# Optimization experiments

Measured on AMD Instinct MI355X. Metric: run time of the kernel, lower is better.

## Reference

```python
import jax, jax.numpy as jnp
import numpy as np

B, H, W, C = 4, 192, 640, 32
S = 32
STEPS = np.arange(S, dtype=np.float32)  # depth steps (init kwarg 'steps')


def setup_inputs() -> dict:
    key = jax.random.key(0)
    k1, k2, k3, k4, k5 = jax.random.split(key, 5)
    x = jax.random.normal(k1, (B, H, W, C), jnp.float32)
    y = jax.random.normal(k2, (B, H, W, C), jnp.float32)
    # principal point near image center, focal ~500px, small translation T12
    origin = jnp.array([[W / 2.0, H / 2.0]], jnp.float32) + jax.random.uniform(k3, (B, 2), jnp.float32)
    focal = 500.0 + 50.0 * jax.random.uniform(k4, (B, 2), jnp.float32)
    T12 = 0.01 * jax.random.normal(k5, (B, 3), jnp.float32)
    return {"x": x, "y": y, "origin": origin, "focal": focal, "T12": T12}


def _bilinear_1img(img, sx, sy):
    # img [H,W,C]; sx [W]: source x-coord for each output column; sy [H]: source y per row.
    # Matches tf.contrib.image.transform BILINEAR with fill value 0 outside the image.
    x0 = jnp.floor(sx); fx = sx - x0
    y0 = jnp.floor(sy); fy = sy - y0
    x0i = x0.astype(jnp.int32); x1i = x0i + 1
    y0i = y0.astype(jnp.int32); y1i = y0i + 1
    mx0 = ((x0i >= 0) & (x0i < W)).astype(img.dtype)
    mx1 = ((x1i >= 0) & (x1i < W)).astype(img.dtype)
    my0 = ((y0i >= 0) & (y0i < H)).astype(img.dtype)
    my1 = ((y1i >= 0) & (y1i < H)).astype(img.dtype)
    # interpolate along y first (transform is separable: x'=a*x+b, y'=a*y+c)
    r0 = img[jnp.clip(y0i, 0, H - 1)]                     # [H,W,C]
    r1 = img[jnp.clip(y1i, 0, H - 1)]                     # [H,W,C]
    rows = (my0 * (1.0 - fy))[:, None, None] * r0 + (my1 * fy)[:, None, None] * r1
    c0 = rows[:, jnp.clip(x0i, 0, W - 1)]                 # [H,W,C]
    c1 = rows[:, jnp.clip(x1i, 0, W - 1)]
    return (mx0 * (1.0 - fx))[None, :, None] * c0 + (mx1 * fx)[None, :, None] * c1


_warp = jax.vmap(lambda img, a, b, c: _bilinear_1img(
    img,
    a * jnp.arange(W, dtype=img.dtype) + b,
    a * jnp.arange(H, dtype=img.dtype) + c))


def reference(x, y, origin, focal, T12):
    tz = T12[:, 2]  # [B]

    def per_step(d):
        safe_d = jnp.where(d == 0.0, 1.0, d)
        D = jnp.where(d == 0.0, 0.0, 1.0 / (1.0 / safe_d + tz))          # [B]
        alpha = 1.0 - D * tz                                              # [B]
        beta = D * tz * origin[:, 0] + D * focal[:, 0] * T12[:, 0]        # [B]
        gamma = D * tz * origin[:, 1] + D * focal[:, 1] * T12[:, 1]       # [B]
        shifted = _warp(x, alpha, beta, gamma)                            # [B,H,W,C]
        return jnp.mean(shifted * y, axis=3)                              # [B,H,W]

    corr = jax.lax.map(jax.checkpoint(per_step), jnp.asarray(STEPS))      # [S,B,H,W]
    return jnp.transpose(corr, (1, 2, 3, 0))                              # [B,H,W,S]
```

## Files before the change

kernel.cpp:

```cpp
#include <hip/hip_runtime.h>
#include <hip/hip_fp16.h>

#define BB 4
#define HH 192
#define WW 640
#define CC 32
#define SS 32
#define PXB 64
#define MAXW 152

typedef _Float16 half2n __attribute__((ext_vector_type(2)));

#if defined(__has_builtin)
#if __has_builtin(__builtin_amdgcn_fdot2)
#define HAS_FDOT2 1
#endif
#endif

__device__ __forceinline__ float fdot2_acc(__half2 a, __half2 b, float acc) {
#ifdef HAS_FDOT2
    return __builtin_amdgcn_fdot2(__builtin_bit_cast(half2n, a),
                                  __builtin_bit_cast(half2n, b), acc, false);
#else
    const float2 af = __half22float2(a);
    const float2 bf = __half22float2(b);
    return acc + af.x * bf.x + af.y * bf.y;
#endif
}

__device__ __forceinline__ unsigned pk2(float w) {
    return (unsigned)__builtin_bit_cast(unsigned short, __float2half_rn(w)) * 0x10001u;
}

__device__ __forceinline__ int swz(int c) { return c ^ ((c >> 2) & 3); }

__global__ __launch_bounds__(256) void convert_x_kernel(const float* __restrict__ x,
                                                        __half* __restrict__ xh) {
    const size_t i = ((size_t)blockIdx.x * 256 + threadIdx.x) * 8;
    const float4 f0 = *(const float4*)(x + i);
    const float4 f1 = *(const float4*)(x + i + 4);
    uint4 u;
    u.x = __builtin_bit_cast(unsigned, __floats2half2_rn(f0.x, f0.y));
    u.y = __builtin_bit_cast(unsigned, __floats2half2_rn(f0.z, f0.w));
    u.z = __builtin_bit_cast(unsigned, __floats2half2_rn(f1.x, f1.y));
    u.w = __builtin_bit_cast(unsigned, __floats2half2_rn(f1.z, f1.w));
    *(uint4*)(xh + i) = u;
}

__global__ __launch_bounds__(256, 8) void corr_kernel(
    const __half* __restrict__ xh, const float* __restrict__ y,
    const float* __restrict__ origin, const float* __restrict__ focal,
    const float* __restrict__ T12, float* __restrict__ out)
{
    __shared__ uint4 sU[SS];
    __shared__ uint4 sV[SS];
    __shared__ uint4 sComb[2][MAXW * 4];

    const int tid  = threadIdx.x;
    const int lane = tid & 63;
    const int wave = tid >> 6;
    const int slot = lane >> 2;
    const int cg   = lane & 3;

    const int p0 = blockIdx.x * PXB;
    const int w0 = p0 % WW;
    const int h  = (p0 / WW) % HH;
    const int b  = p0 / (WW * HH);

    if (tid < SS) {
        const float tz = T12[b * 3 + 2];
        const float kx = tz * origin[b * 2 + 0] + focal[b * 2 + 0] * T12[b * 3 + 0];
        const float ky = tz * origin[b * 2 + 1] + focal[b * 2 + 1] * T12[b * 3 + 1];
        const float sf = (float)tid;
        const float D = sf * __builtin_amdgcn_rcpf(1.0f + sf * tz);
        const float alpha = 1.0f - D * tz;
        const float dkx = D * kx;
        const float dky = D * ky;

        const float syv = alpha * (float)h + dky;
        const float y0f = floorf(syv);
        const float fy  = syv - y0f;
        const int   y0  = (int)y0f;
        const int   y1  = y0 + 1;
        const float wy0 = (y0 >= 0 && y0 < HH) ? (1.0f - fy) : 0.0f;
        const float wy1 = (y1 >= 0 && y1 < HH) ? fy : 0.0f;
        const int   cy0 = min(max(y0, 0), HH - 1);
        const int   cy1 = min(max(y1, 0), HH - 1);

        const float sxa = alpha * (float)w0 + dkx;
        const float sxb = alpha * (float)(w0 + PXB - 1) + dkx;
        const int xlo = (int)floorf(fminf(sxa, sxb));
        const int xhi = (int)floorf(fmaxf(sxa, sxb)) + 1;
        const int width4 = (xhi - xlo + 1) * 4;

        uint4 U, V;
        U.x = __builtin_bit_cast(unsigned, alpha);
        U.y = __builtin_bit_cast(unsigned, dkx);
        U.z = (unsigned)xlo;
        U.w = (unsigned)width4;
        V.x = (unsigned)((cy0 * WW) << 6);
        V.y = (unsigned)((cy1 * WW) << 6);
        V.z = pk2(wy0);
        V.w = pk2(wy1);
        sU[tid] = U;
        sV[tid] = V;
    }

    const int pme = p0 + wave * 16 + slot;
    __half2 yh[4];
    {
        const float4 ya = *(const float4*)(y + (size_t)pme * CC + cg * 8);
        const float4 yb = *(const float4*)(y + (size_t)pme * CC + cg * 8 + 4);
        yh[0] = __floats2half2_rn(ya.x, ya.y);
        yh[1] = __floats2half2_rn(ya.z, ya.w);
        yh[2] = __floats2half2_rn(yb.x, yb.y);
        yh[3] = __floats2half2_rn(yb.z, yb.w);
    }

    const char* xbase = (const char*)(xh + (size_t)b * HH * WW * CC);
    const int cgb = cg * 16;
    const float pxf = (float)(w0 + wave * 16 + slot);
    float* outp = out + (size_t)pme * SS;

    float res[8];

    __syncthreads();

#pragma unroll 1
    for (int g = 0; g < 4; ++g) {
#pragma unroll
        for (int j = 0; j < 8; ++j) {
            const int s = g * 8 + j;
            const uint4 U = sU[s];
            const uint4 V = sV[s];
            const float alpha  = __builtin_bit_cast(float, U.x);
            const float dkx    = __builtin_bit_cast(float, U.y);
            const int   xlo    = (int)U.z;
            const int   width4 = (int)U.w;
            const int   buf    = s & 1;
            const bool  fits   = (width4 <= MAXW * 4);

            if (fits) {
                const __half2 wy0h = __builtin_bit_cast(__half2, V.z);
                const __half2 wy1h = __builtin_bit_cast(__half2, V.w);
                for (int c = tid; c < width4; c += 256) {
                    const int cpx = min(max(xlo + (c >> 2), 0), WW - 1);
                    const unsigned po = (unsigned)((cpx << 6) + ((c & 3) << 4));
                    const uint4 a  = *(const uint4*)(xbase + (size_t)(V.x + po));
                    const uint4 bq = *(const uint4*)(xbase + (size_t)(V.y + po));
                    uint4 o;
#pragma unroll
                    for (int i = 0; i < 4; ++i) {
                        __half2 r = __hmul2(__builtin_bit_cast(__half2, (&a.x)[i]), wy0h);
                        r = __hfma2(__builtin_bit_cast(__half2, (&bq.x)[i]), wy1h, r);
                        (&o.x)[i] = __builtin_bit_cast(unsigned, r);
                    }
                    sComb[buf][swz(c)] = o;
                }
            }
            __syncthreads();

            const float sx  = alpha * pxf + dkx;
            const float x0f = floorf(sx);
            const float fx  = sx - x0f;
            const int   x0  = (int)x0f;
            const int   x1  = x0 + 1;
            const float wx0f = (x0 >= 0 && x0 < WW) ? (1.0f - fx) : 0.0f;
            const float wx1f = (x1 >= 0 && x1 < WW) ? fx : 0.0f;
            const __half2 wx0 = __builtin_bit_cast(__half2, pk2(wx0f));
            const __half2 wx1 = __builtin_bit_cast(__half2, pk2(wx1f));
            const int cx0 = min(max(x0, 0), WW - 1);
            const int cx1 = min(max(x1, 0), WW - 1);

            float acc = 0.0f;
            if (fits) {
                const int wlim = (width4 >> 2) - 1;
                const int l0 = min(max(cx0 - xlo, 0), wlim);
                const int l1 = min(max(cx1 - xlo, 0), wlim);
                const uint4 ca = sComb[buf][swz(l0 * 4 + cg)];
                const uint4 cb = sComb[buf][swz(l1 * 4 + cg)];
#pragma unroll
                for (int i = 0; i < 4; ++i) {
                    __half2 v = __hmul2(__builtin_bit_cast(__half2, (&ca.x)[i]), wx0);
                    v = __hfma2(__builtin_bit_cast(__half2, (&cb.x)[i]), wx1, v);
                    acc = fdot2_acc(v, yh[i], acc);
                }
            } else {
                const __half2 wy0h = __builtin_bit_cast(__half2, V.z);
                const __half2 wy1h = __builtin_bit_cast(__half2, V.w);
                const uint4 a  = *(const uint4*)(xbase + (size_t)(V.x + (unsigned)((cx0 << 6) + cgb)));
                const uint4 bq = *(const uint4*)(xbase + (size_t)(V.x + (unsigned)((cx1 << 6) + cgb)));
                const uint4 c2 = *(const uint4*)(xbase + (size_t)(V.y + (unsigned)((cx0 << 6) + cgb)));
                const uint4 d  = *(const uint4*)(xbase + (size_t)(V.y + (unsigned)((cx1 << 6) + cgb)));
#pragma unroll
                for (int i = 0; i < 4; ++i) {
                    __half2 top = __hmul2(__builtin_bit_cast(__half2, (&a.x)[i]), wx0);
                    top = __hfma2(__builtin_bit_cast(__half2, (&bq.x)[i]), wx1, top);
                    __half2 bot = __hmul2(__builtin_bit_cast(__half2, (&c2.x)[i]), wx0);
                    bot = __hfma2(__builtin_bit_cast(__half2, (&d.x)[i]), wx1, bot);
                    __half2 v = __hmul2(top, wy0h);
                    v = __hfma2(bot, wy1h, v);
                    acc = fdot2_acc(v, yh[i], acc);
                }
            }

            acc += __shfl_xor(acc, 1, 64);
            acc += __shfl_xor(acc, 2, 64);
            if (g == cg) res[j] = acc * (1.0f / 32.0f);
        }
    }

    float4 o0, o1;
    o0.x = res[0]; o0.y = res[1]; o0.z = res[2]; o0.w = res[3];
    o1.x = res[4]; o1.y = res[5]; o1.z = res[6]; o1.w = res[7];
    *(float4*)(outp + cg * 8)     = o0;
    *(float4*)(outp + cg * 8 + 4) = o1;
}

extern "C" void kernel_launch(void* const* d_in, const int* in_sizes, int n_in,
                              void* d_out, int out_size, void* d_ws, size_t ws_size,
                              hipStream_t stream) {
    const float* x = (const float*)d_in[0];
    const float* y = (const float*)d_in[1];
    const float* origin = (const float*)d_in[2];
    const float* focal = (const float*)d_in[3];
    const float* T12 = (const float*)d_in[4];
    float* out = (float*)d_out;
    __half* xh = (__half*)d_ws;

    const int nelem = BB * HH * WW * CC;
    convert_x_kernel<<<nelem / (256 * 8), 256, 0, stream>>>(x, xh);

    const int npix = BB * HH * WW;
    corr_kernel<<<npix / PXB, 256, 0, stream>>>(xh, y, origin, focal, T12, out);
}
```

Before: 314.0 us.

## Map one pixel per lane with single-wave blocks and planar padded LDS

Restructures the correlation kernel so each 64-thread block is a single wave and each lane handles one pixel across all 32 channels. This removes the per-step cross-lane shuffle reductions and the 4-lanes-per-pixel split. The combined-row LDS buffer becomes a padded channel-plane layout, single-buffered with two barriers per step, and MAXW is reduced. The risk is that staging each row into LDS now uses a quarter as many threads, and per-block occupancy changes.

Result: slower. 336.9 us (+7.3%).

```diff
diff --git a/kernel.cpp b/kernel.cpp
--- a/kernel.cpp
+++ b/kernel.cpp
@@ -7,7 +7,8 @@
 #define CC 32
 #define SS 32
 #define PXB 64
-#define MAXW 152
+#define MAXW 140
+#define PLANE (MAXW + 1)
 
 typedef _Float16 half2n __attribute__((ext_vector_type(2)));
 
@@ -17,7 +18,7 @@
 #endif
 #endif
 
-__device__ __forceinline__ float fdot2_acc(__half2 a, __half2 b, float acc) {
+static __device__ __forceinline__ float fdot2_acc(__half2 a, __half2 b, float acc) {
 #ifdef HAS_FDOT2
     return __builtin_amdgcn_fdot2(__builtin_bit_cast(half2n, a),
                                   __builtin_bit_cast(half2n, b), acc, false);
@@ -28,11 +29,9 @@
 #endif
 }
 
-__device__ __forceinline__ unsigned pk2(float w) {
+static __device__ __forceinline__ unsigned pk2(float w) {
     return (unsigned)__builtin_bit_cast(unsigned short, __float2half_rn(w)) * 0x10001u;
 }
-
-__device__ __forceinline__ int swz(int c) { return c ^ ((c >> 2) & 3); }
 
 __global__ __launch_bounds__(256) void convert_x_kernel(const float* __restrict__ x,
                                                         __half* __restrict__ xh) {
@@ -47,31 +46,27 @@
     *(uint4*)(xh + i) = u;
 }
 
-__global__ __launch_bounds__(256, 8) void corr_kernel(
+__global__ __launch_bounds__(64, 4) void corr_kernel(
     const __half* __restrict__ xh, const float* __restrict__ y,
     const float* __restrict__ origin, const float* __restrict__ focal,
     const float* __restrict__ T12, float* __restrict__ out)
 {
     __shared__ uint4 sU[SS];
     __shared__ uint4 sV[SS];
-    __shared__ uint4 sComb[2][MAXW * 4];
-
-    const int tid  = threadIdx.x;
-    const int lane = tid & 63;
-    const int wave = tid >> 6;
-    const int slot = lane >> 2;
-    const int cg   = lane & 3;
+    __shared__ uint4 comb[4][PLANE];
+
+    const int lane = threadIdx.x;
 
     const int p0 = blockIdx.x * PXB;
     const int w0 = p0 % WW;
     const int h  = (p0 / WW) % HH;
     const int b  = p0 / (WW * HH);
 
-    if (tid < SS) {
+    if (lane < SS) {
         const float tz = T12[b * 3 + 2];
         const float kx = tz * origin[b * 2 + 0] + focal[b * 2 + 0] * T12[b * 3 + 0];
         const float ky = tz * origin[b * 2 + 1] + focal[b * 2 + 1] * T12[b * 3 + 1];
-        const float sf = (float)tid;
+        const float sf = (float)lane;
         const float D = sf * __builtin_amdgcn_rcpf(1.0f + sf * tz);
         const float alpha = 1.0f - D * tz;
         const float dkx = D * kx;
@@ -102,32 +97,31 @@
         V.y = (unsigned)((cy1 * WW) << 6);
         V.z = pk2(wy0);
         V.w = pk2(wy1);
-        sU[tid] = U;
-        sV[tid] = V;
+        sU[lane] = U;
+        sV[lane] = V;
     }
 
-    const int pme = p0 + wave * 16 + slot;
-    __half2 yh[4];
+    const int pme = p0 + lane;
+    __half2 yh[16];
     {
-        const float4 ya = *(const float4*)(y + (size_t)pme * CC + cg * 8);
-        const float4 yb = *(const float4*)(y + (size_t)pme * CC + cg * 8 + 4);
-        yh[0] = __floats2half2_rn(ya.x, ya.y);
-        yh[1] = __floats2half2_rn(ya.z, ya.w);
-        yh[2] = __floats2half2_rn(yb.x, yb.y);
-        yh[3] = __floats2half2_rn(yb.z, yb.w);
+        const float4* yp = (const float4*)(y + (size_t)pme * CC);
+#pragma unroll
+        for (int q = 0; q < 8; ++q) {
+            const float4 f = yp[q];
+            yh[2 * q]     = __floats2half2_rn(f.x, f.y);
+            yh[2 * q + 1] = __floats2half2_rn(f.z, f.w);
+        }
     }
 
     const char* xbase = (const char*)(xh + (size_t)b * HH * WW * CC);
-    const int cgb = cg * 16;
-    const float pxf = (float)(w0 + wave * 16 + slot);
+    const float pxf = (float)(w0 + lane);
     float* outp = out + (size_t)pme * SS;
-
-    float res[8];
 
     __syncthreads();
 
 #pragma unroll 1
     for (int g = 0; g < 4; ++g) {
+        float res[8];
 #pragma unroll
         for (int j = 0; j < 8; ++j) {
             const int s = g * 8 + j;
@@ -137,28 +131,7 @@
             const float dkx    = __builtin_bit_cast(float, U.y);
             const int   xlo    = (int)U.z;
             const int   width4 = (int)U.w;
-            const int   buf    = s & 1;
             const bool  fits   = (width4 <= MAXW * 4);
-
-            if (fits) {
-                const __half2 wy0h = __builtin_bit_cast(__half2, V.z);
-                const __half2 wy1h = __builtin_bit_cast(__half2, V.w);
-                for (int c = tid; c < width4; c += 256) {
-                    const int cpx = min(max(xlo + (c >> 2), 0), WW - 1);
-                    const unsigned po = (unsigned)((cpx << 6) + ((c & 3) << 4));
-                    const uint4 a  = *(const uint4*)(xbase + (size_t)(V.x + po));
-                    const uint4 bq = *(const uint4*)(xbase + (size_t)(V.y + po));
-                    uint4 o;
-#pragma unroll
-                    for (int i = 0; i < 4; ++i) {
-                        __half2 r = __hmul2(__builtin_bit_cast(__half2, (&a.x)[i]), wy0h);
-                        r = __hfma2(__builtin_bit_cast(__half2, (&bq.x)[i]), wy1h, r);
-                        (&o.x)[i] = __builtin_bit_cast(unsigned, r);
-                    }
-                    sComb[buf][swz(c)] = o;
-                }
-            }
-            __syncthreads();
 
             const float sx  = alpha * pxf + dkx;
             const float x0f = floorf(sx);
@@ -172,49 +145,80 @@
             const int cx0 = min(max(x0, 0), WW - 1);
             const int cx1 = min(max(x1, 0), WW - 1);
 
+            if (fits) {
+                const __half2 wy0h = __builtin_bit_cast(__half2, V.z);
+                const __half2 wy1h = __builtin_bit_cast(__half2, V.w);
+                for (int c = lane; c < width4; c += 64) {
+                    const int cpx = min(max(xlo + (c >> 2), 0), WW - 1);
+                    const unsigned po = (unsigned)((cpx << 6) + ((c & 3) << 4));
+                    const uint4 a  = *(const uint4*)(xbase + (size_t)(V.x + po));
+                    const uint4 bq = *(const uint4*)(xbase + (size_t)(V.y + po));
+                    uint4 o;
+#pragma unroll
+                    for (int i = 0; i < 4; ++i) {
+                        __half2 r = __hmul2(__builtin_bit_cast(__half2, (&a.x)[i]), wy0h);
+                        r = __hfma2(__builtin_bit_cast(__half2, (&bq.x)[i]), wy1h, r);
+                        (&o.x)[i] = __builtin_bit_cast(unsigned, r);
+                    }
+                    comb[c & 3][c >> 2] = o;
+                }
+            }
+            __syncthreads();
+
             float acc = 0.0f;
             if (fits) {
                 const int wlim = (width4 >> 2) - 1;
                 const int l0 = min(max(cx0 - xlo, 0), wlim);
                 const int l1 = min(max(cx1 - xlo, 0), wlim);
-                const uint4 ca = sComb[buf][swz(l0 * 4 + cg)];
-                const uint4 cb = sComb[buf][swz(l1 * 4 + cg)];
+                const uint4* b0 = &comb[0][l0];
+                const uint4* b1 = &comb[0][l1];
+                uint4 A[4], Bq[4];
 #pragma unroll
                 for (int i = 0; i < 4; ++i) {
-                    __half2 v = __hmul2(__builtin_bit_cast(__half2, (&ca.x)[i]), wx0);
-                    v = __hfma2(__builtin_bit_cast(__half2, (&cb.x)[i]), wx1, v);
-                    acc = fdot2_acc(v, yh[i], acc);
+                    A[i]  = b0[i * PLANE];
+                    Bq[i] = b1[i * PLANE];
+                }
+#pragma unroll
+                for (int i = 0; i < 4; ++i) {
+#pragma unroll
+                    for (int w = 0; w < 4; ++w) {
+                        __half2 v = __hmul2(__builtin_bit_cast(__half2, (&A[i].x)[w]), wx0);
+                        v = __hfma2(__builtin_bit_cast(__half2, (&Bq[i].x)[w]), wx1, v);
+                        acc = fdot2_acc(v, yh[i * 4 + w], acc);
+                    }
                 }
             } else {
                 const __half2 wy0h = __builtin_bit_cast(__half2, V.z);
                 const __half2 wy1h = __builtin_bit_cast(__half2, V.w);
-                const uint4 a  = *(const uint4*)(xbase + (size_t)(V.x + (unsigned)((cx0 << 6) + cgb)));
-                const uint4 bq = *(const uint4*)(xbase + (size_t)(V.x + (unsigned)((cx1 << 6) + cgb)));
-                const uint4 c2 = *(const uint4*)(xbase + (size_t)(V.y + (unsigned)((cx0 << 6) + cgb)));
-                const uint4 d  = *(const uint4*)(xbase + (size_t)(V.y + (unsigned)((cx1 << 6) + cgb)));
+                const uint4* r0p0 = (const uint4*)(xbase + (size_t)(V.x + ((unsigned)cx0 << 6)));
+                const uint4* r0p1 = (const uint4*)(xbase + (size_t)(V.x + ((unsigned)cx1 << 6)));
+                const uint4* r1p0 = (const uint4*)(xbase + (size_t)(V.y + ((unsigned)cx0 << 6)));
+                const uint4* r1p1 = (const uint4*)(xbase + (size_t)(V.y + ((unsigned)cx1 << 6)));
 #pragma unroll
                 for (int i = 0; i < 4; ++i) {
-                    __half2 top = __hmul2(__builtin_bit_cast(__half2, (&a.x)[i]), wx0);
-                    top = __hfma2(__builtin_bit_cast(__half2, (&bq.x)[i]), wx1, top);
-                    __half2 bot = __hmul2(__builtin_bit_cast(__half2, (&c2.x)[i]), wx0);
-                    bot = __hfma2(__builtin_bit_cast(__half2, (&d.x)[i]), wx1, bot);
-                    __half2 v = __hmul2(top, wy0h);
-                    v = __hfma2(bot, wy1h, v);
-                    acc = fdot2_acc(v, yh[i], acc);
+                    const uint4 a  = r0p0[i];
+                    const uint4 bq = r0p1[i];
+                    const uint4 c2 = r1p0[i];
+                    const uint4 d  = r1p1[i];
+#pragma unroll
+                    for (int w = 0; w < 4; ++w) {
+                        __half2 top = __hmul2(__builtin_bit_cast(__half2, (&a.x)[w]), wx0);
+                        top = __hfma2(__builtin_bit_cast(__half2, (&bq.x)[w]), wx1, top);
+                        __half2 bot = __hmul2(__builtin_bit_cast(__half2, (&c2.x)[w]), wx0);
+                        bot = __hfma2(__builtin_bit_cast(__half2, (&d.x)[w]), wx1, bot);
+                        __half2 v = __hmul2(top, wy0h);
+                        v = __hfma2(bot, wy1h, v);
+                        acc = fdot2_acc(v, yh[i * 4 + w], acc);
+                    }
                 }
             }
-
-            acc += __shfl_xor(acc, 1, 64);
-            acc += __shfl_xor(acc, 2, 64);
-            if (g == cg) res[j] = acc * (1.0f / 32.0f);
+            __syncthreads();
+
+            res[j] = acc * (1.0f / 32.0f);
         }
+        *(float4*)(outp + g * 8)     = make_float4(res[0], res[1], res[2], res[3]);
+        *(float4*)(outp + g * 8 + 4) = make_float4(res[4], res[5], res[6], res[7]);
     }
-
-    float4 o0, o1;
-    o0.x = res[0]; o0.y = res[1]; o0.z = res[2]; o0.w = res[3];
-    o1.x = res[4]; o1.y = res[5]; o1.z = res[6]; o1.w = res[7];
-    *(float4*)(outp + cg * 8)     = o0;
-    *(float4*)(outp + cg * 8 + 4) = o1;
 }
 
 extern "C" void kernel_launch(void* const* d_in, const int* in_sizes, int n_in,
@@ -232,5 +236,5 @@
     convert_x_kernel<<<nelem / (256 * 8), 256, 0, stream>>>(x, xh);
 
     const int npix = BB * HH * WW;
-    corr_kernel<<<npix / PXB, 256, 0, stream>>>(xh, y, origin, focal, T12, out);
-}
+    corr_kernel<<<npix / PXB, 64, 0, stream>>>(xh, y, origin, focal, T12, out);
+}
```
